# Kernel tuning notes

Measured on AMD Instinct MI355X. Metric: run time of the kernel, lower is better.

## Reference

```python
import jax, jax.numpy as jnp
import numpy as np

N, E, F_IN, NCLS, H = 50000, 800000, 128, 10, 64


def setup_inputs() -> dict:
    key = jax.random.key(0)
    ks = jax.random.split(key, 24)
    p = lambda k, shp: (jax.random.normal(k, shp, dtype=jnp.float32) * 0.1)
    inp = {
        'x': jax.random.normal(ks[0], (N, F_IN), dtype=jnp.float32),
        'edge_index': jax.random.randint(ks[1], (2, E), 0, N, dtype=jnp.int64),
        'gcn1_W': p(ks[2], (F_IN, 128)), 'gcn1_b': p(ks[3], (128,)),
        'gcn2_W': p(ks[4], (128, 64)),  'gcn2_b': p(ks[5], (64,)),
        'gcn3_W': p(ks[6], (64, 32)),   'gcn3_b': p(ks[7], (32,)),
        'gat_W': p(ks[8], (32, 32)), 'gat_a_src': p(ks[9], (32,)),
        'gat_a_dst': p(ks[10], (32,)), 'gat_b': p(ks[11], (32,)),
        'lstm_Wih_f': p(ks[12], (4 * H, 32)), 'lstm_bih_f': p(ks[13], (4 * H,)), 'lstm_bhh_f': p(ks[14], (4 * H,)),
        'lstm_Wih_b': p(ks[15], (4 * H, 32)), 'lstm_bih_b': p(ks[16], (4 * H,)), 'lstm_bhh_b': p(ks[17], (4 * H,)),
        'bn_gamma': jnp.ones((2 * H,), jnp.float32), 'bn_beta': jnp.zeros((2 * H,), jnp.float32),
        'fc_W': p(ks[18], (NCLS, 2 * H)), 'fc_b': p(ks[19], (NCLS,)),
    }
    return inp


def _forward(x, edge_index, gcn1_W, gcn1_b, gcn2_W, gcn2_b, gcn3_W, gcn3_b,
             gat_W, gat_a_src, gat_a_dst, gat_b,
             lstm_Wih_f, lstm_bih_f, lstm_bhh_f, lstm_Wih_b, lstm_bih_b, lstm_bhh_b,
             bn_gamma, bn_beta, fc_W, fc_b):
    n = x.shape[0]
    loop = jnp.arange(n)
    row = jnp.concatenate([edge_index[0], loop])  # source nodes (+ self loops)
    col = jnp.concatenate([edge_index[1], loop])  # target nodes
    deg = jax.ops.segment_sum(jnp.ones_like(col, dtype=x.dtype), col, num_segments=n)
    dis = jax.lax.rsqrt(jnp.maximum(deg, 1e-12))  # deg >= 1 due to self loops
    norm = dis[row] * dis[col]

    def gcn(h, W, b):
        h = h @ W
        return jax.ops.segment_sum(h[row] * norm[:, None], col, num_segments=n) + b

    h = jax.nn.relu(gcn(x, gcn1_W, gcn1_b))
    h = jax.nn.relu(gcn(h, gcn2_W, gcn2_b))
    h = gcn(h, gcn3_W, gcn3_b)

    # GAT (1 head), self loops already in row/col, softmax over incoming edges per target
    g = h @ gat_W
    e = jax.nn.leaky_relu((g @ gat_a_src)[row] + (g @ gat_a_dst)[col], negative_slope=0.2)
    m = jax.ops.segment_max(e, col, num_segments=n)
    ee = jnp.exp(e - m[col])
    att = ee / jax.ops.segment_sum(ee, col, num_segments=n)[col]
    h = jax.ops.segment_sum(g[row] * att[:, None], col, num_segments=n) + gat_b
    h = jax.nn.relu(h)

    # bidirectional LSTM with seq_len=1, h0=c0=0 -> single cell step per direction
    def lstm_dir(xx, Wih, bih, bhh):
        gt = xx @ Wih.T + bih + bhh
        i, f, c, o = jnp.split(gt, 4, axis=-1)  # torch gate order i,f,g,o
        return jax.nn.sigmoid(o) * jnp.tanh(jax.nn.sigmoid(i) * jnp.tanh(c))

    r = jnp.concatenate([lstm_dir(h, lstm_Wih_f, lstm_bih_f, lstm_bhh_f),
                         lstm_dir(h, lstm_Wih_b, lstm_bih_b, lstm_bhh_b)], axis=-1)
    # eval mode: dropout = identity; BatchNorm1d with running_mean=0, running_var=1
    r = r * (bn_gamma / jnp.sqrt(jnp.float32(1.0 + 1e-5))) + bn_beta
    return r @ fc_W.T + fc_b


def reference(x, edge_index, gcn1_W, gcn1_b, gcn2_W, gcn2_b, gcn3_W, gcn3_b,
              gat_W, gat_a_src, gat_a_dst, gat_b,
              lstm_Wih_f, lstm_bih_f, lstm_bhh_f, lstm_Wih_b, lstm_bih_b, lstm_bhh_b,
              bn_gamma, bn_beta, fc_W, fc_b):
    return _forward(x, edge_index, gcn1_W, gcn1_b, gcn2_W, gcn2_b, gcn3_W, gcn3_b,
                    gat_W, gat_a_src, gat_a_dst, gat_b,
                    lstm_Wih_f, lstm_bih_f, lstm_bhh_f, lstm_Wih_b, lstm_bih_b, lstm_bhh_b,
                    bn_gamma, bn_beta, fc_W, fc_b)
```

## Files before the change

kernel.cpp:

```cpp
#include <hip/hip_runtime.h>
#include <hip/hip_bf16.h>
#include <math.h>

typedef __hip_bfloat16 bf16;

#define NN 50000
#define EE 800000
#define EPB 4096
#define NBK 196
#define BCAP 6144

__device__ __forceinline__ float b2f(bf16 v) { return __bfloat162float(v); }
__device__ __forceinline__ float rcp_(float x) { return __builtin_amdgcn_rcpf(x); }
__device__ __forceinline__ float sigmoidf_(float x) { return rcp_(1.0f + __expf(-x)); }
__device__ __forceinline__ float tanhf_(float x) {
    float xx = fminf(fmaxf(x, -15.0f), 15.0f);
    float e = __expf(2.0f * xx);
    return (e - 1.0f) * rcp_(e + 1.0f);
}
__device__ __forceinline__ float leakyf_(float x) { return x > 0.0f ? x : 0.2f * x; }
__device__ __forceinline__ unsigned short f2bf(float f) {
    unsigned u = __float_as_uint(f);
    unsigned r = (u + 0x7FFFu + ((u >> 16) & 1u)) >> 16;
    return (unsigned short)r;
}
__device__ __forceinline__ unsigned pack2(float a, float b) {
    return (unsigned)f2bf(a) | ((unsigned)f2bf(b) << 16);
}
__device__ __forceinline__ float lo_(unsigned u) { return __uint_as_float(u << 16); }
__device__ __forceinline__ float hi_(unsigned u) { return __uint_as_float(u & 0xFFFF0000u); }

#define OFF_W1 0
#define OFF_B1 16384
#define OFF_W2 16512
#define OFF_B2 24704
#define OFF_W3 24768
#define OFF_B3 26816
#define OFF_GATW 26848
#define OFF_GAS 27872
#define OFF_GAD 27904
#define OFF_GAB 27936
#define OFF_WIHF 27968
#define OFF_BIHF 36160
#define OFF_BHHF 36416
#define OFF_WIHB 36672
#define OFF_BIHB 44864
#define OFF_BHHB 45120
#define OFF_GAMMA 45376
#define OFF_BETA 45504
#define OFF_FCW 45632
#define OFF_FCB 46912
#define WTOTAL 46922

struct WSrc { const void* p[20]; };

__global__ void k_detect(const unsigned short* __restrict__ xraw,
                         const unsigned int* __restrict__ eraw, int* __restrict__ flags) {
    __shared__ int f32f, i64f;
    int t = threadIdx.x;
    if (t == 0) { f32f = 0; i64f = 1; }
    __syncthreads();
    for (int i = t; i < 4096; i += 256) {
        unsigned short u = xraw[i];
        int ex = (u >> 7) & 0xFF;
        if (ex >= 0xC0) atomicOr(&f32f, 1);
        if (eraw[2 * i + 1] != 0u) atomicAnd(&i64f, 0);
    }
    __syncthreads();
    if (t == 0) { flags[0] = f32f; flags[1] = i64f; }
}

__global__ void k_cvt_w(WSrc srcs, float* __restrict__ dst, const int* __restrict__ flags,
                        int total) {
    constexpr int WOFF[21] = {OFF_W1,   OFF_B1,   OFF_W2,   OFF_B2,   OFF_W3,   OFF_B3,
                              OFF_GATW, OFF_GAS,  OFF_GAD,  OFF_GAB,  OFF_WIHF, OFF_BIHF,
                              OFF_BHHF, OFF_WIHB, OFF_BIHB, OFF_BHHB, OFF_GAMMA, OFF_BETA,
                              OFF_FCW,  OFF_FCB,  WTOTAL};
    int i = blockIdx.x * 256 + threadIdx.x;
    if (i >= total) return;
    int tn = 0;
#pragma unroll
    for (int j = 1; j < 20; ++j)
        if (i >= WOFF[j]) tn = j;
    int local = i - WOFF[tn];
    if (flags[0]) dst[i] = ((const float*)srcs.p[tn])[local];
    else dst[i] = b2f(((const bf16*)srcs.p[tn])[local]);
}

__global__ __launch_bounds__(256) void k_hist(const void* __restrict__ eraw,
                                              unsigned* __restrict__ gh,
                                              const int* __restrict__ flags) {
    __shared__ int h[256];
    int t = threadIdx.x, b = blockIdx.x;
    h[t] = 0;
    __syncthreads();
    int e0 = b * EPB;
    bool i64 = flags[1] != 0;
    for (int i = t; i < EPB; i += 256) {
        int e = e0 + i;
        if (e < EE) {
            int d = i64 ? (int)((const long long*)eraw)[EE + e] : ((const int*)eraw)[EE + e];
            d = min(max(d, 0), NN - 1);
            atomicAdd(&h[d >> 8], 1);
        }
    }
    __syncthreads();
    gh[b * 256 + t] = (unsigned)h[t];
}

__global__ __launch_bounds__(256) void k_bscan(const unsigned* __restrict__ gh,
                                               unsigned* __restrict__ gh2,
                                               int* __restrict__ bb, int* __restrict__ rptr) {
    __shared__ int s[256];
    int t = threadIdx.x;
    unsigned run = 0;
    for (int blk = 0; blk < NBK; ++blk) {
        unsigned v = gh[blk * 256 + t];
        gh2[blk * 256 + t] = run;
        run += v;
    }
    s[t] = (int)run;
    __syncthreads();
    for (int o = 1; o < 256; o <<= 1) {
        int x = (t >= o) ? s[t - o] : 0;
        __syncthreads();
        s[t] += x;
        __syncthreads();
    }
    bb[t] = s[t] - (int)run;
    if (t == 0) rptr[NN] = EE;
}

__global__ __launch_bounds__(256) void k_scatter(const void* __restrict__ eraw,
                                                 const unsigned* __restrict__ gh2,
                                                 const int* __restrict__ bb,
                                                 int2* __restrict__ ebkt,
                                                 const int* __restrict__ flags) {
    __shared__ unsigned cur[256];
    int t = threadIdx.x, b = blockIdx.x;
    cur[t] = gh2[b * 256 + t] + (unsigned)bb[t];
    __syncthreads();
    int e0 = b * EPB;
    bool i64 = flags[1] != 0;
    for (int i = t; i < EPB; i += 256) {
        int e = e0 + i;
        if (e < EE) {
            int sn, d;
            if (i64) {
                sn = (int)((const long long*)eraw)[e];
                d = (int)((const long long*)eraw)[EE + e];
            } else {
                sn = ((const int*)eraw)[e];
                d = ((const int*)eraw)[EE + e];
            }
            sn = min(max(sn, 0), NN - 1);
            d = min(max(d, 0), NN - 1);
            unsigned pos = atomicAdd(&cur[d >> 8], 1u);
            if (pos < (unsigned)EE) ebkt[pos] = make_int2(sn, d);
        }
    }
}

__global__ __launch_bounds__(256) void k_bucket_csr(const int2* __restrict__ ebkt,
                                                    const int* __restrict__ bb,
                                                    int* __restrict__ rptr,
                                                    float* __restrict__ dis,
                                                    int* __restrict__ csr_src) {
    __shared__ int hist[256];
    __shared__ int excl[256];
    __shared__ int cur[256];
    __shared__ int sorted[BCAP];
    int t = threadIdx.x, b = blockIdx.x;
    int s0 = bb[b], s1 = bb[b + 1];
    int len = min(s1 - s0, BCAP);
    hist[t] = 0;
    __syncthreads();
    for (int i = t; i < len; i += 256) atomicAdd(&hist[ebkt[s0 + i].y & 255], 1);
    __syncthreads();
    int v = hist[t];
    excl[t] = v;
    __syncthreads();
    for (int o = 1; o < 256; o <<= 1) {
        int x = (t >= o) ? excl[t - o] : 0;
        __syncthreads();
        excl[t] += x;
        __syncthreads();
    }
    int loc = excl[t] - v;
    int node = b * 256 + t;
    if (node < NN) {
        rptr[node] = s0 + loc;
        dis[node] = rsqrtf((float)(v + 1));
    }
    cur[t] = loc;
    __syncthreads();
    for (int i = t; i < len; i += 256) {
        int2 p = ebkt[s0 + i];
        int pos = atomicAdd(&cur[p.y & 255], 1);
        if (pos < BCAP) sorted[pos] = p.x;
    }
    __syncthreads();
    for (int i = t; i < len; i += 256) csr_src[s0 + i] = sorted[i];
}

template <int KIN, int KOUT, int MODE, bool SCALE>
__global__ __launch_bounds__(256) void k_tile_mm(const void* __restrict__ A,
                                                 const float* __restrict__ W,
                                                 unsigned* __restrict__ C, int n,
                                                 const int* __restrict__ flags, int want,
                                                 const float* __restrict__ dis) {
    if (want >= 0 && flags[0] != want) return;
    constexpr int BK = 32;
    constexpr int AST = BK + 4;
    constexpr int CPT = KOUT / 16;
    __shared__ float As[64 * AST];
    __shared__ float Ws[BK * KOUT];
    int t = threadIdx.x;
    int jc = t & 15;
    int ng = t >> 4;
    int base = blockIdx.x * 64;
    float acc[4][CPT];
#pragma unroll
    for (int i = 0; i < 4; ++i)
#pragma unroll
        for (int c = 0; c < CPT; ++c) acc[i][c] = 0.f;
    int snode = t >> 2;
    int gnode = min(base + snode, n - 1);
    int koff = (t & 3) * 8;
    for (int k0 = 0; k0 < KIN; k0 += BK) {
        {
            const float4* src = (const float4*)(W + k0 * KOUT);
            float4* dst = (float4*)Ws;
#pragma unroll
            for (int p = 0; p < BK * KOUT / 1024; ++p) dst[t + p * 256] = src[t + p * 256];
        }
        if (MODE == 0) {
            const unsigned* xr = (const unsigned*)A + (size_t)gnode * (KIN / 2) + (k0 + koff) / 2;
            unsigned u0 = xr[0], u1 = xr[1], u2 = xr[2], u3 = xr[3];
            float* d = As + snode * AST + koff;
            d[0] = lo_(u0); d[1] = hi_(u0);
            d[2] = lo_(u1); d[3] = hi_(u1);
            d[4] = lo_(u2); d[5] = hi_(u2);
            d[6] = lo_(u3); d[7] = hi_(u3);
        } else {
            const float4* ar = (const float4*)((const float*)A + (size_t)gnode * KIN + k0 + koff);
            float4 v0 = ar[0], v1 = ar[1];
            float4* d = (float4*)(As + snode * AST + koff);
            d[0] = v0;
            d[1] = v1;
        }
        __syncthreads();
#pragma unroll 8
        for (int k = 0; k < BK; ++k) {
            float w[CPT];
            const float* wr = Ws + k * KOUT + jc * CPT;
            if constexpr (CPT >= 4) {
#pragma unroll
                for (int c = 0; c < CPT; c += 4) {
                    float4 wv = *(const float4*)(wr + c);
                    w[c] = wv.x; w[c + 1] = wv.y; w[c + 2] = wv.z; w[c + 3] = wv.w;
                }
            } else {
                float2 wv = *(const float2*)wr;
                w[0] = wv.x; w[1] = wv.y;
            }
            float a0 = As[(ng * 4 + 0) * AST + k];
            float a1 = As[(ng * 4 + 1) * AST + k];
            float a2 = As[(ng * 4 + 2) * AST + k];
            float a3 = As[(ng * 4 + 3) * AST + k];
#pragma unroll
            for (int c = 0; c < CPT; ++c) {
                acc[0][c] += a0 * w[c];
                acc[1][c] += a1 * w[c];
                acc[2][c] += a2 * w[c];
                acc[3][c] += a3 * w[c];
            }
        }
        __syncthreads();
    }
#pragma unroll
    for (int i = 0; i < 4; ++i) {
        int node = base + ng * 4 + i;
        if (node < n) {
            float sc = SCALE ? dis[node] : 1.0f;
            unsigned* cr = C + (size_t)node * (KOUT / 2) + jc * (CPT / 2);
#pragma unroll
            for (int c = 0; c < CPT; c += 2)
                cr[c / 2] = pack2(acc[i][c] * sc, acc[i][c + 1] * sc);
        }
    }
}

template <bool RELU>
__global__ void k_agg128(const unsigned* __restrict__ t, const int* __restrict__ rptr,
                         const int* __restrict__ csr_src, const float* __restrict__ dis,
                         const float* __restrict__ bias, float* __restrict__ out, int n) {
    int wave = (blockIdx.x * blockDim.x + threadIdx.x) >> 6;
    int lane = threadIdx.x & 63;
    if (wave >= n) return;
    int dst = wave;
    float dd = dis[dst];
    float ax, ay;
    {
        unsigned u = t[(size_t)dst * 64 + lane];
        ax = lo_(u);
        ay = hi_(u);
    }
    int s = __builtin_amdgcn_readfirstlane(max(0, min(rptr[dst], EE)));
    int e = __builtin_amdgcn_readfirstlane(max(s, min(rptr[dst + 1], EE)));
    int j = s;
    for (; j + 8 <= e; j += 8) {
        int i0 = csr_src[j], i1 = csr_src[j + 1], i2 = csr_src[j + 2], i3 = csr_src[j + 3];
        int i4 = csr_src[j + 4], i5 = csr_src[j + 5], i6 = csr_src[j + 6], i7 = csr_src[j + 7];
        unsigned u0 = t[(size_t)i0 * 64 + lane], u1 = t[(size_t)i1 * 64 + lane];
        unsigned u2 = t[(size_t)i2 * 64 + lane], u3 = t[(size_t)i3 * 64 + lane];
        unsigned u4 = t[(size_t)i4 * 64 + lane], u5 = t[(size_t)i5 * 64 + lane];
        unsigned u6 = t[(size_t)i6 * 64 + lane], u7 = t[(size_t)i7 * 64 + lane];
        ax += (lo_(u0) + lo_(u1)) + (lo_(u2) + lo_(u3)) + (lo_(u4) + lo_(u5)) + (lo_(u6) + lo_(u7));
        ay += (hi_(u0) + hi_(u1)) + (hi_(u2) + hi_(u3)) + (hi_(u4) + hi_(u5)) + (hi_(u6) + hi_(u7));
    }
    for (; j + 4 <= e; j += 4) {
        int i0 = csr_src[j], i1 = csr_src[j + 1], i2 = csr_src[j + 2], i3 = csr_src[j + 3];
        unsigned u0 = t[(size_t)i0 * 64 + lane], u1 = t[(size_t)i1 * 64 + lane];
        unsigned u2 = t[(size_t)i2 * 64 + lane], u3 = t[(size_t)i3 * 64 + lane];
        ax += (lo_(u0) + lo_(u1)) + (lo_(u2) + lo_(u3));
        ay += (hi_(u0) + hi_(u1)) + (hi_(u2) + hi_(u3));
    }
    for (; j < e; ++j) {
        unsigned u0 = t[(size_t)csr_src[j] * 64 + lane];
        ax += lo_(u0);
        ay += hi_(u0);
    }
    float2 bv = *(const float2*)(bias + 2 * lane);
    float vx = ax * dd + bv.x;
    float vy = ay * dd + bv.y;
    if (RELU) { vx = fmaxf(vx, 0.f); vy = fmaxf(vy, 0.f); }
    *(float2*)(out + (size_t)dst * 128 + 2 * lane) = make_float2(vx, vy);
}

template <bool RELU>
__global__ void k_agg64(const unsigned* __restrict__ t, const int* __restrict__ rptr,
                        const int* __restrict__ csr_src, const float* __restrict__ dis,
                        const float* __restrict__ bias, float* __restrict__ out, int n) {
    int wave = (blockIdx.x * blockDim.x + threadIdx.x) >> 6;
    int lane = threadIdx.x & 63;
    if (wave >= n) return;
    int dst = wave;
    int half = lane >> 5, l32 = lane & 31;
    float dd = dis[dst];
    float ax = 0.f, ay = 0.f;
    if (!half) {
        unsigned u = t[(size_t)dst * 32 + l32];
        ax = lo_(u);
        ay = hi_(u);
    }
    int s = max(0, min(rptr[dst], EE));
    int e = max(s, min(rptr[dst + 1], EE));
    int cnt = e - s;
    int pairs = cnt >> 1;
    int p = 0;
    for (; p + 4 <= pairs; p += 4) {
        int jb = s + 2 * p + half;
        int i0 = csr_src[jb], i1 = csr_src[jb + 2], i2 = csr_src[jb + 4], i3 = csr_src[jb + 6];
        unsigned u0 = t[(size_t)i0 * 32 + l32], u1 = t[(size_t)i1 * 32 + l32];
        unsigned u2 = t[(size_t)i2 * 32 + l32], u3 = t[(size_t)i3 * 32 + l32];
        ax += (lo_(u0) + lo_(u1)) + (lo_(u2) + lo_(u3));
        ay += (hi_(u0) + hi_(u1)) + (hi_(u2) + hi_(u3));
    }
    for (; p < pairs; ++p) {
        int i0 = csr_src[s + 2 * p + half];
        unsigned u0 = t[(size_t)i0 * 32 + l32];
        ax += lo_(u0);
        ay += hi_(u0);
    }
    if ((cnt & 1) && !half) {
        unsigned u0 = t[(size_t)csr_src[e - 1] * 32 + l32];
        ax += lo_(u0);
        ay += hi_(u0);
    }
    ax += __shfl_down(ax, 32);
    ay += __shfl_down(ay, 32);
    if (!half) {
        float2 bv = *(const float2*)(bias + 2 * l32);
        float vx = ax * dd + bv.x;
        float vy = ay * dd + bv.y;
        if (RELU) { vx = fmaxf(vx, 0.f); vy = fmaxf(vy, 0.f); }
        *(float2*)(out + (size_t)dst * 64 + 2 * l32) = make_float2(vx, vy);
    }
}

template <bool RELU>
__global__ void k_agg32(const unsigned* __restrict__ t, const int* __restrict__ rptr,
                        const int* __restrict__ csr_src, const float* __restrict__ dis,
                        const float* __restrict__ bias, float* __restrict__ out, int n) {
    int wave = (blockIdx.x * blockDim.x + threadIdx.x) >> 6;
    int lane = threadIdx.x & 63;
    if (wave >= n) return;
    int dst = wave;
    int q = lane >> 4, l16 = lane & 15;
    float dd = dis[dst];
    float ax = 0.f, ay = 0.f;
    if (q == 0) {
        unsigned u = t[(size_t)dst * 16 + l16];
        ax = lo_(u);
        ay = hi_(u);
    }
    int s = max(0, min(rptr[dst], EE));
    int e = max(s, min(rptr[dst + 1], EE));
    int cnt = e - s;
    int quads = cnt >> 2;
    int p = 0;
    for (; p + 4 <= quads; p += 4) {
        int jb = s + 4 * p + q;
        int i0 = csr_src[jb], i1 = csr_src[jb + 4], i2 = csr_src[jb + 8], i3 = csr_src[jb + 12];
        unsigned u0 = t[(size_t)i0 * 16 + l16], u1 = t[(size_t)i1 * 16 + l16];
        unsigned u2 = t[(size_t)i2 * 16 + l16], u3 = t[(size_t)i3 * 16 + l16];
        ax += (lo_(u0) + lo_(u1)) + (lo_(u2) + lo_(u3));
        ay += (hi_(u0) + hi_(u1)) + (hi_(u2) + hi_(u3));
    }
    for (; p < quads; ++p) {
        int i0 = csr_src[s + 4 * p + q];
        unsigned u0 = t[(size_t)i0 * 16 + l16];
        ax += lo_(u0);
        ay += hi_(u0);
    }
    int rem = cnt - 4 * quads;
    if (q < rem) {
        unsigned u0 = t[(size_t)csr_src[s + 4 * quads + q] * 16 + l16];
        ax += lo_(u0);
        ay += hi_(u0);
    }
    ax += __shfl_down(ax, 32);
    ay += __shfl_down(ay, 32);
    ax += __shfl_down(ax, 16);
    ay += __shfl_down(ay, 16);
    if (q == 0) {
        float2 bv = *(const float2*)(bias + 2 * l16);
        float vx = ax * dd + bv.x;
        float vy = ay * dd + bv.y;
        if (RELU) { vx = fmaxf(vx, 0.f); vy = fmaxf(vy, 0.f); }
        *(float2*)(out + (size_t)dst * 32 + 2 * l16) = make_float2(vx, vy);
    }
}

__global__ void k_gat_vec(const unsigned* __restrict__ g, const float* __restrict__ a_src,
                          const float* __restrict__ a_dst, float* __restrict__ asrc,
                          float* __restrict__ adst, int n) {
    int i = blockIdx.x * 256 + threadIdx.x;
    if (i >= n) return;
    float s = 0.0f, d = 0.0f;
    const unsigned* gr = g + (size_t)i * 16;
#pragma unroll
    for (int k = 0; k < 16; ++k) {
        unsigned u = gr[k];
        float v0 = lo_(u), v1 = hi_(u);
        s += v0 * a_src[2 * k] + v1 * a_src[2 * k + 1];
        d += v0 * a_dst[2 * k] + v1 * a_dst[2 * k + 1];
    }
    asrc[i] = s;
    adst[i] = d;
}

__global__ void k_gat_agg(const unsigned* __restrict__ g, const int* __restrict__ rptr,
                          const int* __restrict__ csr_src, const float* __restrict__ asrc,
                          const float* __restrict__ adst, const float* __restrict__ gat_b,
                          float* __restrict__ out, int n) {
    int wave = (blockIdx.x * blockDim.x + threadIdx.x) >> 6;
    int lane = threadIdx.x & 63;
    if (wave >= n) return;
    int dst = wave;
    int q = lane >> 4, l16 = lane & 15;
    float ad = adst[dst];
    int s = max(0, min(rptr[dst], EE));
    int e = max(s, min(rptr[dst + 1], EE));
    float ax = 0.f, ay = 0.f, denom = 0.f;
    if (q == 0) {
        float w0 = __expf(fminf(leakyf_(asrc[dst] + ad), 80.f));
        unsigned u = g[(size_t)dst * 16 + l16];
        ax = lo_(u) * w0;
        ay = hi_(u) * w0;
        denom = w0;
    }
    int cnt = e - s;
    int quads = cnt >> 2;
    int p = 0;
    for (; p + 4 <= quads; p += 4) {
        int jb = s + 4 * p + q;
        int i0 = csr_src[jb], i1 = csr_src[jb + 4], i2 = csr_src[jb + 8], i3 = csr_src[jb + 12];
        float a0 = asrc[i0], a1 = asrc[i1], a2 = asrc[i2], a3 = asrc[i3];
        unsigned u0 = g[(size_t)i0 * 16 + l16], u1 = g[(size_t)i1 * 16 + l16];
        unsigned u2 = g[(size_t)i2 * 16 + l16], u3 = g[(size_t)i3 * 16 + l16];
        float w0 = __expf(fminf(leakyf_(a0 + ad), 80.f));
        float w1 = __expf(fminf(leakyf_(a1 + ad), 80.f));
        float w2 = __expf(fminf(leakyf_(a2 + ad), 80.f));
        float w3 = __expf(fminf(leakyf_(a3 + ad), 80.f));
        denom += (w0 + w1) + (w2 + w3);
        ax += lo_(u0) * w0 + lo_(u1) * w1 + lo_(u2) * w2 + lo_(u3) * w3;
        ay += hi_(u0) * w0 + hi_(u1) * w1 + hi_(u2) * w2 + hi_(u3) * w3;
    }
    for (; p < quads; ++p) {
        int i0 = csr_src[s + 4 * p + q];
        float wgt = __expf(fminf(leakyf_(asrc[i0] + ad), 80.f));
        unsigned u0 = g[(size_t)i0 * 16 + l16];
        denom += wgt;
        ax += lo_(u0) * wgt;
        ay += hi_(u0) * wgt;
    }
    int rem = cnt - 4 * quads;
    if (q < rem) {
        int i0 = csr_src[s + 4 * quads + q];
        float wgt = __expf(fminf(leakyf_(asrc[i0] + ad), 80.f));
        unsigned u0 = g[(size_t)i0 * 16 + l16];
        denom += wgt;
        ax += lo_(u0) * wgt;
        ay += hi_(u0) * wgt;
    }
    ax += __shfl_down(ax, 32);
    ay += __shfl_down(ay, 32);
    denom += __shfl_down(denom, 32);
    ax += __shfl_down(ax, 16);
    ay += __shfl_down(ay, 16);
    denom += __shfl_down(denom, 16);
    if (q == 0) {
        float r = rcp_(denom);
        float vx = fmaxf(ax * r + gat_b[2 * l16], 0.f);
        float vy = fmaxf(ay * r + gat_b[2 * l16 + 1], 0.f);
        *(float2*)(out + (size_t)dst * 32 + 2 * l16) = make_float2(vx, vy);
    }
}

__global__ __launch_bounds__(128) void k_lstm_fc(const float* __restrict__ h,
                                                 const float* __restrict__ wp,
                                                 void* __restrict__ out,
                                                 const int* __restrict__ flags, int n) {
    __shared__ float hs[32 * 32];
    __shared__ float rs[32 * 129];
    __shared__ float fcw[1280];
    __shared__ float ps[32 * 40];
    int t = threadIdx.x;
    int base = blockIdx.x * 32;
    for (int idx = t; idx < 256; idx += 128) {
        int nd = idx >> 3, k4 = idx & 7;
        int node = min(base + nd, n - 1);
        ((float4*)hs)[idx] = ((const float4*)(h + (size_t)node * 32))[k4];
    }
    for (int i = t; i < 1280; i += 128) fcw[i] = wp[OFF_FCW + i];
    __syncthreads();
    {
        int dir = t >> 6, j = t & 63;
        const float* W = wp + (dir ? OFF_WIHB : OFF_WIHF);
        const float* bi = wp + (dir ? OFF_BIHB : OFF_BIHF);
        const float* bh = wp + (dir ? OFF_BHHB : OFF_BHHF);
        float wi[32], wc[32], wo[32];
#pragma unroll
        for (int k = 0; k < 32; ++k) {
            wi[k] = W[j * 32 + k];
            wc[k] = W[(128 + j) * 32 + k];
            wo[k] = W[(192 + j) * 32 + k];
        }
        float bI = bi[j] + bh[j];
        float bC = bi[128 + j] + bh[128 + j];
        float bO = bi[192 + j] + bh[192 + j];
        float gsc = wp[OFF_GAMMA + t] * rsqrtf(1.0f + 1e-5f);
        float gbe = wp[OFF_BETA + t];
#pragma unroll 2
        for (int nn = 0; nn < 32; ++nn) {
            const float* hv = hs + nn * 32;
            float ai = bI, ac = bC, ao = bO;
#pragma unroll
            for (int k = 0; k < 32; ++k) {
                float hk = hv[k];
                ai += hk * wi[k];
                ac += hk * wc[k];
                ao += hk * wo[k];
            }
            float v = sigmoidf_(ao) * tanhf_(sigmoidf_(ai) * tanhf_(ac));
            rs[nn * 129 + t] = v * gsc + gbe;
        }
    }
    __syncthreads();
    {
        int nd = t & 31, q = t >> 5;
        float p10[10];
#pragma unroll
        for (int c = 0; c < 10; ++c) p10[c] = 0.f;
#pragma unroll
        for (int k = 0; k < 32; ++k) {
            float rv = rs[nd * 129 + q * 32 + k];
#pragma unroll
            for (int c = 0; c < 10; ++c) p10[c] += rv * fcw[c * 128 + q * 32 + k];
        }
#pragma unroll
        for (int c = 0; c < 10; ++c) ps[nd * 40 + q * 10 + c] = p10[c];
    }
    __syncthreads();
    for (int idx = t; idx < 320; idx += 128) {
        int nd = idx / 10, c = idx % 10;
        int node = base + nd;
        if (node < n) {
            float v = wp[OFF_FCB + c] + ps[nd * 40 + c] + ps[nd * 40 + 10 + c] +
                      ps[nd * 40 + 20 + c] + ps[nd * 40 + 30 + c];
            if (flags[0]) ((float*)out)[(size_t)node * 10 + c] = v;
            else ((bf16*)out)[(size_t)node * 10 + c] = __float2bfloat16(v);
        }
    }
}

extern "C" void kernel_launch(void* const* d_in, const int* in_sizes, int n_in,
                              void* d_out, int out_size, void* d_ws, size_t ws_size,
                              hipStream_t stream) {
    const int N = NN;

    char* w = (char*)d_ws;
    auto alloc = [&](size_t bytes) {
        void* p = (void*)w;
        w += (bytes + 255) & ~(size_t)255;
        return p;
    };
    int* flags = (int*)alloc(256);
    float* wpool = (float*)alloc((size_t)WTOTAL * 4);
    float* dis = (float*)alloc((size_t)N * 4);
    int* rptr = (int*)alloc((size_t)(N + 1) * 4);
    int* csr_src = (int*)alloc((size_t)EE * 4);
    unsigned* gh = (unsigned*)alloc((size_t)NBK * 256 * 4);
    unsigned* gh2 = (unsigned*)alloc((size_t)NBK * 256 * 4);
    int* bb = (int*)alloc(1024);
    int2* ebkt = (int2*)alloc((size_t)EE * 8);
    float* asrc = (float*)alloc((size_t)N * 4);
    float* adst = (float*)alloc((size_t)N * 4);
    unsigned* bufT = (unsigned*)alloc((size_t)N * 64 * 4);
    float* bufH = (float*)alloc((size_t)N * 128 * 4);

    WSrc ws_srcs;
    for (int i = 0; i < 20; ++i) ws_srcs.p[i] = d_in[2 + i];

    const int NB = (N + 255) / 256;
    const int AGG = (N + 3) / 4;
    const int TMB = (N + 63) / 64;
    const int LFB = (N + 31) / 32;
    const int WB = (WTOTAL + 255) / 256;

    k_detect<<<1, 256, 0, stream>>>((const unsigned short*)d_in[0],
                                    (const unsigned int*)d_in[1], flags);
    k_cvt_w<<<WB, 256, 0, stream>>>(ws_srcs, wpool, flags, WTOTAL);
    k_hist<<<NBK, 256, 0, stream>>>(d_in[1], gh, flags);
    k_bscan<<<1, 256, 0, stream>>>(gh, gh2, bb, rptr);
    k_scatter<<<NBK, 256, 0, stream>>>(d_in[1], gh2, bb, ebkt, flags);
    k_bucket_csr<<<NBK, 256, 0, stream>>>(ebkt, bb, rptr, dis, csr_src);

    k_tile_mm<128, 128, 0, true><<<TMB, 256, 0, stream>>>(d_in[0], wpool + OFF_W1, bufT, N, flags, 0, dis);
    k_tile_mm<128, 128, 1, true><<<TMB, 256, 0, stream>>>(d_in[0], wpool + OFF_W1, bufT, N, flags, 1, dis);
    k_agg128<true><<<AGG, 256, 0, stream>>>(bufT, rptr, csr_src, dis, wpool + OFF_B1, bufH, N);
    k_tile_mm<128, 64, 1, true><<<TMB, 256, 0, stream>>>(bufH, wpool + OFF_W2, bufT, N, flags, -1, dis);
    k_agg64<true><<<AGG, 256, 0, stream>>>(bufT, rptr, csr_src, dis, wpool + OFF_B2, bufH, N);
    k_tile_mm<64, 32, 1, true><<<TMB, 256, 0, stream>>>(bufH, wpool + OFF_W3, bufT, N, flags, -1, dis);
    k_agg32<false><<<AGG, 256, 0, stream>>>(bufT, rptr, csr_src, dis, wpool + OFF_B3, bufH, N);
    k_tile_mm<32, 32, 1, false><<<TMB, 256, 0, stream>>>(bufH, wpool + OFF_GATW, bufT, N, flags, -1, dis);
    k_gat_vec<<<NB, 256, 0, stream>>>(bufT, wpool + OFF_GAS, wpool + OFF_GAD, asrc, adst, N);
    k_gat_agg<<<AGG, 256, 0, stream>>>(bufT, rptr, csr_src, asrc, adst, wpool + OFF_GAB, bufH, N);
    k_lstm_fc<<<LFB, 128, 0, stream>>>(bufH, wpool, d_out, flags, N);
}
```

Before: 376.6 us.

## Restructure LSTM+FC kernel to keep node features in registers and stream weights

The LSTM/FC tail kernel now gives each thread one node with its 32 input features in registers. The four wavefronts each split the work by direction and half of the hidden units, and read the weights as wave-uniform scalar loads instead of holding 96 weights per thread. The FC projection is fused into the per-hidden-unit loop, which removes the rs/fcw shared staging and two barriers. Blocks grow to 64 nodes and 256 threads, and output writes become contiguous. The trade-off is far more global/scalar weight loads per node, with the weights shared through cache rather than registers.

```diff
diff --git a/kernel.cpp b/kernel.cpp
--- a/kernel.cpp
+++ b/kernel.cpp
@@ -529,79 +529,72 @@
     }
 }
 
-__global__ __launch_bounds__(128) void k_lstm_fc(const float* __restrict__ h,
+__global__ __launch_bounds__(256) void k_lstm_fc(const float* __restrict__ h,
                                                  const float* __restrict__ wp,
                                                  void* __restrict__ out,
                                                  const int* __restrict__ flags, int n) {
-    __shared__ float hs[32 * 32];
-    __shared__ float rs[32 * 129];
-    __shared__ float fcw[1280];
-    __shared__ float ps[32 * 40];
+    __shared__ float ps[4 * 640];
     int t = threadIdx.x;
-    int base = blockIdx.x * 32;
-    for (int idx = t; idx < 256; idx += 128) {
-        int nd = idx >> 3, k4 = idx & 7;
-        int node = min(base + nd, n - 1);
-        ((float4*)hs)[idx] = ((const float4*)(h + (size_t)node * 32))[k4];
-    }
-    for (int i = t; i < 1280; i += 128) fcw[i] = wp[OFF_FCW + i];
-    __syncthreads();
+    int nd = t & 63;
+    int part = __builtin_amdgcn_readfirstlane(t >> 6);
+    int dir = part >> 1, jh = part & 1;
+    int base = blockIdx.x * 64;
+    int node = min(base + nd, n - 1);
+
+    float hv[32];
     {
-        int dir = t >> 6, j = t & 63;
-        const float* W = wp + (dir ? OFF_WIHB : OFF_WIHF);
-        const float* bi = wp + (dir ? OFF_BIHB : OFF_BIHF);
-        const float* bh = wp + (dir ? OFF_BHHB : OFF_BHHF);
-        float wi[32], wc[32], wo[32];
+        const float4* hr = (const float4*)(h + (size_t)node * 32);
+#pragma unroll
+        for (int qq = 0; qq < 8; ++qq) {
+            float4 v = hr[qq];
+            hv[4 * qq + 0] = v.x;
+            hv[4 * qq + 1] = v.y;
+            hv[4 * qq + 2] = v.z;
+            hv[4 * qq + 3] = v.w;
+        }
+    }
+
+    const float* W = wp + (dir ? OFF_WIHB : OFF_WIHF);
+    const float* bi = wp + (dir ? OFF_BIHB : OFF_BIHF);
+    const float* bh = wp + (dir ? OFF_BHHB : OFF_BHHF);
+    const float* fcw = wp + OFF_FCW;
+    float p10[10];
+#pragma unroll
+    for (int c = 0; c < 10; ++c) p10[c] = 0.f;
+
+    int j0 = jh * 32;
+#pragma unroll 2
+    for (int j = j0; j < j0 + 32; ++j) {
+        const float* wi = W + (size_t)j * 32;
+        const float* wc = W + (size_t)(128 + j) * 32;
+        const float* wo = W + (size_t)(192 + j) * 32;
+        float ai = bi[j] + bh[j];
+        float ac = bi[128 + j] + bh[128 + j];
+        float ao = bi[192 + j] + bh[192 + j];
 #pragma unroll
         for (int k = 0; k < 32; ++k) {
-            wi[k] = W[j * 32 + k];
-            wc[k] = W[(128 + j) * 32 + k];
-            wo[k] = W[(192 + j) * 32 + k];
-        }
-        float bI = bi[j] + bh[j];
-        float bC = bi[128 + j] + bh[128 + j];
-        float bO = bi[192 + j] + bh[192 + j];
-        float gsc = wp[OFF_GAMMA + t] * rsqrtf(1.0f + 1e-5f);
-        float gbe = wp[OFF_BETA + t];
-#pragma unroll 2
-        for (int nn = 0; nn < 32; ++nn) {
-            const float* hv = hs + nn * 32;
-            float ai = bI, ac = bC, ao = bO;
-#pragma unroll
-            for (int k = 0; k < 32; ++k) {
-                float hk = hv[k];
-                ai += hk * wi[k];
-                ac += hk * wc[k];
-                ao += hk * wo[k];
-            }
-            float v = sigmoidf_(ao) * tanhf_(sigmoidf_(ai) * tanhf_(ac));
-            rs[nn * 129 + t] = v * gsc + gbe;
-        }
-    }
-    __syncthreads();
-    {
-        int nd = t & 31, q = t >> 5;
-        float p10[10];
-#pragma unroll
-        for (int c = 0; c < 10; ++c) p10[c] = 0.f;
-#pragma unroll
-        for (int k = 0; k < 32; ++k) {
-            float rv = rs[nd * 129 + q * 32 + k];
-#pragma unroll
-            for (int c = 0; c < 10; ++c) p10[c] += rv * fcw[c * 128 + q * 32 + k];
-        }
-#pragma unroll
-        for (int c = 0; c < 10; ++c) ps[nd * 40 + q * 10 + c] = p10[c];
-    }
-    __syncthreads();
-    for (int idx = t; idx < 320; idx += 128) {
-        int nd = idx / 10, c = idx % 10;
-        int node = base + nd;
-        if (node < n) {
-            float v = wp[OFF_FCB + c] + ps[nd * 40 + c] + ps[nd * 40 + 10 + c] +
-                      ps[nd * 40 + 20 + c] + ps[nd * 40 + 30 + c];
-            if (flags[0]) ((float*)out)[(size_t)node * 10 + c] = v;
-            else ((bf16*)out)[(size_t)node * 10 + c] = __float2bfloat16(v);
+            float hk = hv[k];
+            ai += hk * wi[k];
+            ac += hk * wc[k];
+            ao += hk * wo[k];
+        }
+        float v = sigmoidf_(ao) * tanhf_(sigmoidf_(ai) * tanhf_(ac));
+        int jj = dir * 64 + j;
+        float r = v * (wp[OFF_GAMMA + jj] * rsqrtf(1.0f + 1e-5f)) + wp[OFF_BETA + jj];
+#pragma unroll
+        for (int c = 0; c < 10; ++c) p10[c] += r * fcw[c * 128 + jj];
+    }
+#pragma unroll
+    for (int c = 0; c < 10; ++c) ps[part * 640 + nd * 10 + c] = p10[c];
+    __syncthreads();
+    bool f32o = flags[0] != 0;
+    for (int idx = t; idx < 640; idx += 256) {
+        int gnode = base + idx / 10;
+        if (gnode < n) {
+            int c = idx % 10;
+            float v = wp[OFF_FCB + c] + ps[idx] + ps[640 + idx] + ps[1280 + idx] + ps[1920 + idx];
+            if (f32o) ((float*)out)[(size_t)base * 10 + idx] = v;
+            else ((unsigned short*)out)[(size_t)base * 10 + idx] = f2bf(v);
         }
     }
 }
@@ -637,7 +630,7 @@
     const int NB = (N + 255) / 256;
     const int AGG = (N + 3) / 4;
     const int TMB = (N + 63) / 64;
-    const int LFB = (N + 31) / 32;
+    const int LFB = (N + 63) / 64;
     const int WB = (WTOTAL + 255) / 256;
 
     k_detect<<<1, 256, 0, stream>>>((const unsigned short*)d_in[0],
@@ -658,5 +651,5 @@
     k_tile_mm<32, 32, 1, false><<<TMB, 256, 0, stream>>>(bufH, wpool + OFF_GATW, bufT, N, flags, -1, dis);
     k_gat_vec<<<NB, 256, 0, stream>>>(bufT, wpool + OFF_GAS, wpool + OFF_GAD, asrc, adst, N);
     k_gat_agg<<<AGG, 256, 0, stream>>>(bufT, rptr, csr_src, asrc, adst, wpool + OFF_GAB, bufH, N);
-    k_lstm_fc<<<LFB, 128, 0, stream>>>(bufH, wpool, d_out, flags, N);
-}
+    k_lstm_fc<<<LFB, 256, 0, stream>>>(bufH, wpool, d_out, flags, N);
+}
```

Result: no change. 382.9 us (+1.7%).
